# Kernel tuning notes

Measured on AMD Instinct MI355X. Metric: run time of the kernel, lower is better.

Reference implementation:

```python
import jax, jax.numpy as jnp
import numpy as np

# Static configuration (from init_kwargs)
B, T, SP = 4, 100, 20          # batch, max_time_patches, max_space_patches
S = T * SP                      # flattened seq len = 2000
H, NH = 512, 8                  # hidden size, heads
D = H // NH                     # head dim = 64
CF, CB = 4, 4                   # context_forward, context_backward
ROPE_BASE = 10000.0
NEG = -1e9


def setup_inputs() -> dict:
    key = jax.random.key(0)
    ks = jax.random.split(key, 8)
    w = 1.0 / np.sqrt(H)
    x = jax.random.normal(ks[0], (B, S, H), jnp.float32)
    # token order is space-major: timestamps = time-patch id repeated per space patch
    timestamps = jnp.broadcast_to(jnp.tile(jnp.arange(T, dtype=jnp.int32), SP), (B, S))
    attn_mask = jnp.ones((B, S), jnp.int32)
    Wq = jax.random.normal(ks[1], (H, H), jnp.float32) * w
    Wk = jax.random.normal(ks[2], (H, H), jnp.float32) * w
    Wv = jax.random.normal(ks[3], (H, H), jnp.float32) * w
    Wo = jax.random.normal(ks[4], (H, H), jnp.float32) * w
    z = jnp.zeros((H,), jnp.float32)
    return {"x": x, "attn_mask": attn_mask, "timestamps": timestamps,
            "Wq": Wq, "bq": z, "Wk": Wk, "bk": z, "Wv": Wv, "bv": z,
            "Wo": Wo, "bo": z}


def _rotate_half(u):
    return jnp.concatenate((-u[..., D // 2:], u[..., :D // 2]), axis=-1)


def _rope_tables():
    inv_freq = 1.0 / (ROPE_BASE ** (jnp.arange(0, D, 2, dtype=jnp.float32) / D))
    t = jnp.arange(T, dtype=jnp.float32)
    freqs = t[:, None] * inv_freq[None, :]          # [T, D/2]
    emb = jnp.concatenate((freqs, freqs), axis=-1)  # [T, D]
    return jnp.cos(emb), jnp.sin(emb)


def _context_mask():
    # forward/backward banded window in time, tiled over space patches
    ones = jnp.ones((T, T), jnp.float32)
    m = jnp.triu(ones, k=-CF).T          # allow up to CF future time patches
    if CB > 0:
        m = m * jnp.triu(ones, k=-CB)    # allow up to CB past time patches
    return jnp.tile(m, (SP, SP))         # [S, S]


def reference(x, attn_mask, timestamps, Wq, bq, Wk, bk, Wv, bv, Wo, bo):
    # projections -> [B, NH, S, D]
    def heads(w, b):
        return (x @ w + b).reshape(B, S, NH, D).transpose(0, 2, 1, 3)
    q, k, v = heads(Wq, bq), heads(Wk, bk), heads(Wv, bv)

    # rotary position embedding indexed by time-patch timestamps
    cos_t, sin_t = _rope_tables()
    cos = cos_t[timestamps][:, None]     # [B, 1, S, D]
    sin = sin_t[timestamps][:, None]
    q = q * cos + _rotate_half(q) * sin
    k = k * cos + _rotate_half(k) * sin

    # banded-context masked attention
    scores = jnp.einsum('bhqd,bhkd->bhqk', q, k) / jnp.sqrt(jnp.float32(D))
    mask = (_context_mask()[None, None, :, :] *
            attn_mask[:, None, None, :].astype(jnp.float32)) > 0
    scores = jnp.where(mask, scores, NEG)
    attn = jax.nn.softmax(scores, axis=-1)
    out = jnp.einsum('bhqk,bhkd->bhqd', attn, v)
    out = out.transpose(0, 2, 1, 3).reshape(B, S, H)
    return out @ Wo + bo
```

## Files before the change

### kernel.cpp

```cpp
#include <hip/hip_runtime.h>
#include <hip/hip_bf16.h>
#include <stdint.h>


typedef __bf16 bf16x8 __attribute__((ext_vector_type(8)));
typedef float f32x4 __attribute__((ext_vector_type(4)));

static const size_t O_XB = 0;
static const size_t O_WT = 8192000;
static const size_t O_Q  = 10289152;
static const size_t O_K  = 18481152;
static const size_t O_V  = 26673152;
static const size_t O_RC = 34865152;
static const size_t O_RS = 34877952;

__device__ inline void gload16(const void* g, void* l) {
  __builtin_amdgcn_global_load_lds((const __attribute__((address_space(1))) void*)g,
                                   (__attribute__((address_space(3))) void*)l, 16, 0, 0);
}

__device__ inline int xcd_swz(int orig, int nwg) {
  const int q8 = nwg >> 3, r8 = nwg & 7;
  const int xcd = orig & 7;
  return (xcd < r8 ? xcd * (q8 + 1) : r8 * (q8 + 1) + (xcd - r8) * q8) + (orig >> 3);
}

__global__ __launch_bounds__(256) void prep_kernel(
    const float* __restrict__ x, const float* __restrict__ Wq, const float* __restrict__ Wk,
    const float* __restrict__ Wv, const float* __restrict__ Wo,
    __bf16* __restrict__ xb, __bf16* __restrict__ wt,
    float* __restrict__ ropeC, float* __restrict__ ropeS)
{
  __shared__ float tile[64][65];
  const int tid = threadIdx.x;
  const int bx = blockIdx.x;
  if (bx < 4000) {
    const int idx = bx * 256 + tid;
    float4 v = ((const float4*)x)[idx];
    union { ushort4 u; __bf16 b[4]; } p;
    p.b[0] = (__bf16)v.x; p.b[1] = (__bf16)v.y; p.b[2] = (__bf16)v.z; p.b[3] = (__bf16)v.w;
    ((ushort4*)xb)[idx] = p.u;
    return;
  }
  const int wb = bx - 4000;
  const int mat = wb >> 6, sub = wb & 63;
  const int tk = (sub >> 3) * 64, tn = (sub & 7) * 64;
  const float* W = (mat == 0) ? Wq : (mat == 1) ? Wk : (mat == 2) ? Wv : Wo;
#pragma unroll
  for (int it = 0; it < 16; ++it) {
    const int idx = it * 256 + tid;
    const int kl = idx >> 6, nl = idx & 63;
    tile[kl][nl] = W[(size_t)(tk + kl) * 512 + tn + nl];
  }
  __syncthreads();
#pragma unroll
  for (int it = 0; it < 16; ++it) {
    const int idx = it * 256 + tid;
    const int nl = idx >> 6, kl = idx & 63;
    wt[(size_t)mat * 262144 + (size_t)(tn + nl) * 512 + tk + kl] = (__bf16)tile[kl][nl];
  }
  if (wb == 0) {
    for (int idx = tid; idx < 3200; idx += 256) {
      const int t = idx >> 5, i = idx & 31;
      const float f = (float)t * powf(10000.0f, -(float)i / 32.0f);
      ropeC[idx] = cosf(f);
      ropeS[idx] = sinf(f);
    }
  }
}

__device__ inline void mfma_step(const __bf16* ab, const __bf16* bb,
                                 f32x4 (&acc)[4][4], int wm, int wn, int lr, int g)
{
  bf16x8 af[4], bfr[4];
#pragma unroll
  for (int f = 0; f < 4; ++f) {
    af[f]  = *(const bf16x8*)(ab + (wm + f * 16 + lr) * 32 + g * 8);
    bfr[f] = *(const bf16x8*)(bb + (wn + f * 16 + lr) * 32 + g * 8);
  }
#pragma unroll
  for (int i = 0; i < 4; ++i)
#pragma unroll
    for (int j = 0; j < 4; ++j)
      acc[i][j] = __builtin_amdgcn_mfma_f32_16x16x32_bf16(af[i], bfr[j], acc[i][j], 0, 0, 0);
}

__device__ inline void gemm_core_p2(const __bf16* __restrict__ A, const __bf16* __restrict__ Bm,
                                    __bf16* As, __bf16* Bs, f32x4 (&acc)[4][4],
                                    int m0, int n0, int tid, int wm, int wn, int lr, int g)
{
  const int r0 = tid >> 2;
  const int aq = tid & 3;
  int gm0 = m0 + r0;      if (gm0 > 7999) gm0 = 7999;
  int gm1 = m0 + r0 + 64; if (gm1 > 7999) gm1 = 7999;
  const __bf16* a0 = A + (size_t)gm0 * 512 + aq * 8;
  const __bf16* a1 = A + (size_t)gm1 * 512 + aq * 8;
  const __bf16* b0 = Bm + (size_t)(n0 + r0) * 512 + aq * 8;
  const __bf16* b1 = Bm + (size_t)(n0 + r0 + 64) * 512 + aq * 8;

#define STAGE_QK(J, BUF) do {                                      \
    gload16(a0 + (J) * 32, As + (BUF) * 4096 + tid * 8);           \
    gload16(a1 + (J) * 32, As + (BUF) * 4096 + tid * 8 + 2048);    \
    gload16(b0 + (J) * 32, Bs + (BUF) * 4096 + tid * 8);           \
    gload16(b1 + (J) * 32, Bs + (BUF) * 4096 + tid * 8 + 2048);    \
  } while (0)

  STAGE_QK(0, 0);
  STAGE_QK(1, 1);
  __syncthreads();

  int cur = 0, st = 2;
  for (int k = 0; k < 14; ++k) {
    STAGE_QK(k + 2, st);
    mfma_step(As + cur * 4096, Bs + cur * 4096, acc, wm, wn, lr, g);
    asm volatile("s_waitcnt vmcnt(4)" ::: "memory");
    __builtin_amdgcn_s_barrier();
    __builtin_amdgcn_sched_barrier(0);
    if (++cur == 3) cur = 0;
    if (++st == 3) st = 0;
  }
  mfma_step(As + 2 * 4096, Bs + 2 * 4096, acc, wm, wn, lr, g);
  asm volatile("s_waitcnt vmcnt(0)" ::: "memory");
  __builtin_amdgcn_s_barrier();
  __builtin_amdgcn_sched_barrier(0);
  mfma_step(As, Bs, acc, wm, wn, lr, g);
#undef STAGE_QK
}

__global__ __launch_bounds__(256) void qkv_gemm(
    const __bf16* __restrict__ xb, const __bf16* __restrict__ wt,
    const float* __restrict__ bq, const float* __restrict__ bk, const float* __restrict__ bv,
    const float* __restrict__ ropeC, const float* __restrict__ ropeS,
    __bf16* __restrict__ qws, __bf16* __restrict__ kws, __bf16* __restrict__ vws)
{
  const int tid = threadIdx.x;
  const int wgid = xcd_swz(blockIdx.x, 756);
  const int mt = wgid / 12;
  const int rest = wgid - mt * 12;
  const int mat = rest >> 2;
  const int nt = rest & 3;
  const int m0 = mt * 128, n0 = nt * 128;
  __shared__ __bf16 As[12288], Bs[12288];
  __shared__ int posTbl[128];
  f32x4 acc[4][4] = {};
  const int wid = tid >> 6, lane = tid & 63;
  const int wm = (wid >> 1) << 6, wn = (wid & 1) << 6;
  const int lr = lane & 15, g = lane >> 4;

  if (tid < 128) {
    int m = m0 + tid; if (m > 7999) m = 7999;
    const int b = m / 2000;
    const int s = m - b * 2000;
    const int t = s % 100;
    const int sp = s / 100;
    posTbl[tid] = ((b * 16000 + t * 20 + sp) << 7) | t;
  }

  gemm_core_p2(xb, wt + (size_t)mat * 262144, As, Bs, acc, m0, n0, tid, wm, wn, lr, g);

  const int hn = (n0 + wn) >> 6;
  const float* bias = (mat == 0) ? bq : (mat == 1) ? bk : bv;
  __bf16* outp = (mat == 0) ? qws : (mat == 1) ? kws : vws;
  const float qscale = (mat == 0) ? 0.125f : 1.0f;

#pragma unroll
  for (int i = 0; i < 4; ++i) {
#pragma unroll
    for (int r = 0; r < 4; ++r) {
      const int row = wm + i * 16 + g * 4 + r;
      const int m = m0 + row;
      if (m >= 8000) continue;
      const int pk = posTbl[row];
      const int t = pk & 127;
      const size_t ob = ((size_t)((pk >> 7) + hn * 2000)) * 64;
      if (mat == 2) {
#pragma unroll
        for (int j = 0; j < 4; ++j) {
          float v = acc[i][j][r] + bias[n0 + wn + j * 16 + lr];
          outp[ob + j * 16 + lr] = (__bf16)v;
        }
      } else {
#pragma unroll
        for (int j = 0; j < 2; ++j) {
          const int dlo = j * 16 + lr;
          const float alo = acc[i][j][r]     + bias[n0 + wn + j * 16 + lr];
          const float ahi = acc[i][j + 2][r] + bias[n0 + wn + (j + 2) * 16 + lr];
          const float cs = ropeC[t * 32 + dlo], sn = ropeS[t * 32 + dlo];
          const float olo = (alo * cs - ahi * sn) * qscale;
          const float ohi = (ahi * cs + alo * sn) * qscale;
          outp[ob + dlo]      = (__bf16)olo;
          outp[ob + dlo + 32] = (__bf16)ohi;
        }
      }
    }
  }
}

__global__ __launch_bounds__(256) void attn_kernel(
    const __bf16* __restrict__ qw, const __bf16* __restrict__ kw, const __bf16* __restrict__ vw,
    const int* __restrict__ amask, __bf16* __restrict__ aout)
{
  const int wid = threadIdx.x >> 6, lane = threadIdx.x & 63;
  const int tid = threadIdx.x;
  const int lr = lane & 15, g = lane >> 4;
  const int tq = blockIdx.x * 4 + wid;
  const int h = blockIdx.y, b = blockIdx.z;

  int t0 = tq - 4; if (t0 < 0) t0 = 0;
  int t1 = tq + 4; if (t1 > 99) t1 = 99;
  const int k0 = t0 * 20;
  const int nk = (t1 - t0 + 1) * 20;
  const int basew = k0 & ~7;

  const int tq0 = blockIdx.x * 4;
  int t0b = tq0 - 4; if (t0b < 0) t0b = 0;
  int t1b = tq0 + 7; if (t1b > 99) t1b = 99;
  const int kb0 = (t0b * 20) & ~7;
  const int nks = (t1b + 1) * 20 - kb0;
  const int woff = basew - kb0;

  __shared__ __bf16 Vs[64][264];
  __shared__ __bf16 Pl[4][20][200];
  __shared__ float addm[4][192];

  const size_t hb = (size_t)(b * 8 + h) * 2000;
  const __bf16* qp = qw + (hb + (size_t)tq * 20) * 64;
  const __bf16* vp = vw + (hb + (size_t)kb0) * 64;

  for (int k = lane; k < 192; k += 64) {
    const int kg = basew + k;
    float v = -1e9f;
    if (kg >= k0 && kg < k0 + nk) {
      const int tk = kg / 20;
      const int spk = kg - tk * 20;
      if (amask[b * 2000 + spk * 100 + tk] != 0) v = 0.0f;
    }
    addm[wid][k] = v;
  }

  for (int idx = tid; idx < 264 * 16; idx += 256) {
    const int pr = idx >> 4, d4 = (idx & 15) * 4;
    union { ushort4 u; __bf16 e[4]; } p;
    p.u = make_ushort4(0, 0, 0, 0);
    if (pr < nks) p.u = *(const ushort4*)(vp + (size_t)pr * 64 + d4);
    Vs[d4 + 0][pr] = p.e[0];
    Vs[d4 + 1][pr] = p.e[1];
    Vs[d4 + 2][pr] = p.e[2];
    Vs[d4 + 3][pr] = p.e[3];
  }

  bf16x8 qf[2][2];
#pragma unroll
  for (int jq = 0; jq < 2; ++jq) {
    int q = jq * 16 + lr; if (q > 19) q = 19;
#pragma unroll
    for (int ks = 0; ks < 2; ++ks)
      qf[jq][ks] = *(const bf16x8*)(qp + q * 64 + ks * 32 + g * 8);
  }

  f32x4 acc[12][2] = {};
  __builtin_amdgcn_s_setprio(1);
#pragma unroll
  for (int i = 0; i < 12; ++i) {
    int krow = basew + i * 16 + lr; if (krow > 1999) krow = 1999;
    const __bf16* kr = kw + (hb + (size_t)krow) * 64;
    const bf16x8 af0 = *(const bf16x8*)(kr + g * 8);
    const bf16x8 af1 = *(const bf16x8*)(kr + 32 + g * 8);
    acc[i][0] = __builtin_amdgcn_mfma_f32_16x16x32_bf16(af0, qf[0][0], acc[i][0], 0, 0, 0);
    acc[i][0] = __builtin_amdgcn_mfma_f32_16x16x32_bf16(af1, qf[0][1], acc[i][0], 0, 0, 0);
    acc[i][1] = __builtin_amdgcn_mfma_f32_16x16x32_bf16(af0, qf[1][0], acc[i][1], 0, 0, 0);
    acc[i][1] = __builtin_amdgcn_mfma_f32_16x16x32_bf16(af1, qf[1][1], acc[i][1], 0, 0, 0);
  }
  __builtin_amdgcn_s_setprio(0);

  __syncthreads();

#pragma unroll
  for (int jq = 0; jq < 2; ++jq) {
    float mx = -1e30f;
#pragma unroll
    for (int i = 0; i < 12; ++i)
#pragma unroll
      for (int r = 0; r < 4; ++r) {
        acc[i][jq][r] += addm[wid][i * 16 + g * 4 + r];
        mx = fmaxf(mx, acc[i][jq][r]);
      }
    mx = fmaxf(mx, __shfl_xor(mx, 16));
    mx = fmaxf(mx, __shfl_xor(mx, 32));
    float sm = 0.0f;
#pragma unroll
    for (int i = 0; i < 12; ++i)
#pragma unroll
      for (int r = 0; r < 4; ++r) {
        const float p = __expf(acc[i][jq][r] - mx);
        acc[i][jq][r] = p;
        sm += p;
      }
    sm += __shfl_xor(sm, 16);
    sm += __shfl_xor(sm, 32);
    const float rinv = 1.0f / sm;
    const int q = jq * 16 + lr;
    if (q < 20) {
#pragma unroll
      for (int i = 0; i < 12; ++i) {
        union { ushort4 u; __bf16 e[4]; } pk;
        pk.e[0] = (__bf16)(acc[i][jq][0] * rinv);
        pk.e[1] = (__bf16)(acc[i][jq][1] * rinv);
        pk.e[2] = (__bf16)(acc[i][jq][2] * rinv);
        pk.e[3] = (__bf16)(acc[i][jq][3] * rinv);
        *(ushort4*)&Pl[wid][q][i * 16 + g * 4] = pk.u;
      }
    }
  }

  __syncthreads();

  f32x4 acc2[2][4] = {};
  __builtin_amdgcn_s_setprio(1);
#pragma unroll
  for (int kb = 0; kb < 6; ++kb) {
    const int kvloc = woff + kb * 32 + g * 8;
    bf16x8 bfv[4];
#pragma unroll
    for (int j2 = 0; j2 < 4; ++j2)
      bfv[j2] = *(const bf16x8*)&Vs[j2 * 16 + lr][kvloc];
#pragma unroll
    for (int i2 = 0; i2 < 2; ++i2) {
      int qr = i2 * 16 + lr; if (qr > 19) qr = 19;
      const bf16x8 pa = *(const bf16x8*)&Pl[wid][qr][kb * 32 + g * 8];
#pragma unroll
      for (int j2 = 0; j2 < 4; ++j2)
        acc2[i2][j2] = __builtin_amdgcn_mfma_f32_16x16x32_bf16(pa, bfv[j2], acc2[i2][j2], 0, 0, 0);
    }
  }
  __builtin_amdgcn_s_setprio(0);

#pragma unroll
  for (int i2 = 0; i2 < 2; ++i2)
#pragma unroll
    for (int r = 0; r < 4; ++r) {
      const int q = i2 * 16 + g * 4 + r;
      if (q < 20) {
        const size_t ob = ((size_t)b * 2000 + q * 100 + tq) * 512 + h * 64;
#pragma unroll
        for (int j2 = 0; j2 < 4; ++j2)
          aout[ob + j2 * 16 + lr] = (__bf16)acc2[i2][j2][r];
      }
    }
}

__global__ __launch_bounds__(256) void out_gemm(
    const __bf16* __restrict__ ab, const __bf16* __restrict__ wot,
    const float* __restrict__ bo, float* __restrict__ out)
{
  const int tid = threadIdx.x;
  const int wgid = xcd_swz(blockIdx.x, 252);
  const int mt = wgid >> 2, nt = wgid & 3;
  const int m0 = mt * 128, n0 = nt * 128;
  __shared__ __bf16 As[12288], Bs[12288];
  f32x4 acc[4][4] = {};
  const int wid = tid >> 6, lane = tid & 63;
  const int wm = (wid >> 1) << 6, wn = (wid & 1) << 6;
  const int lr = lane & 15, g = lane >> 4;

  gemm_core_p2(ab, wot, As, Bs, acc, m0, n0, tid, wm, wn, lr, g);

#pragma unroll
  for (int i = 0; i < 4; ++i) {
#pragma unroll
    for (int r = 0; r < 4; ++r) {
      const int m = m0 + wm + i * 16 + g * 4 + r;
      if (m < 8000) {
#pragma unroll
        for (int j = 0; j < 4; ++j) {
          const int n = n0 + wn + j * 16 + lr;
          out[(size_t)m * 512 + n] = acc[i][j][r] + bo[n];
        }
      }
    }
  }
}

extern "C" void kernel_launch(void* const* d_in, const int* in_sizes, int n_in,
                              void* d_out, int out_size, void* d_ws, size_t ws_size,
                              hipStream_t stream) {
  const float* x   = (const float*)d_in[0];
  const int* amask = (const int*)d_in[1];
  const float* Wq = (const float*)d_in[3];
  const float* bq = (const float*)d_in[4];
  const float* Wk = (const float*)d_in[5];
  const float* bk = (const float*)d_in[6];
  const float* Wv = (const float*)d_in[7];
  const float* bv = (const float*)d_in[8];
  const float* Wo = (const float*)d_in[9];
  const float* bo = (const float*)d_in[10];
  float* out = (float*)d_out;

  char* ws = (char*)d_ws;
  __bf16* xb    = (__bf16*)(ws + O_XB);
  __bf16* wt    = (__bf16*)(ws + O_WT);
  __bf16* qws   = (__bf16*)(ws + O_Q);
  __bf16* kws   = (__bf16*)(ws + O_K);
  __bf16* vws   = (__bf16*)(ws + O_V);
  float*  ropeC = (float*)(ws + O_RC);
  float*  ropeS = (float*)(ws + O_RS);
  __bf16* aout  = (__bf16*)(ws + O_XB);

  prep_kernel<<<4256, 256, 0, stream>>>(x, Wq, Wk, Wv, Wo, xb, wt, ropeC, ropeS);
  qkv_gemm<<<756, 256, 0, stream>>>(xb, wt, bq, bk, bv, ropeC, ropeS, qws, kws, vws);
  attn_kernel<<<dim3(25, 8, 4), 256, 0, stream>>>(qws, kws, vws, amask, aout);
  out_gemm<<<252, 256, 0, stream>>>(aout, wt + 3 * 262144, bo, out);
}
```

Baseline: 88.08 us.

## Fuse Q/K/V projections per A tile and widen output GEMM tiles

The QKV GEMM now loads each 64-row activation tile once and multiplies it against all three weight matrices, using 500 workgroups instead of 756 that each reloaded the A tile for one matrix. The output GEMM switches to 128x256 tiles with 126 workgroups. Both drop the 3-stage pipeline with partial vmcnt waits in favour of simple double buffering with a full barrier per k-step. That may expose more load latency, and the smaller grids (126 blocks for out_gemm) may underfill the 256 CUs.

```diff
diff --git a/kernel.cpp b/kernel.cpp
--- a/kernel.cpp
+++ b/kernel.cpp
@@ -69,86 +69,26 @@
   }
 }
 
-__device__ inline void mfma_step(const __bf16* ab, const __bf16* bb,
-                                 f32x4 (&acc)[4][4], int wm, int wn, int lr, int g)
-{
-  bf16x8 af[4], bfr[4];
-#pragma unroll
-  for (int f = 0; f < 4; ++f) {
-    af[f]  = *(const bf16x8*)(ab + (wm + f * 16 + lr) * 32 + g * 8);
-    bfr[f] = *(const bf16x8*)(bb + (wn + f * 16 + lr) * 32 + g * 8);
-  }
-#pragma unroll
-  for (int i = 0; i < 4; ++i)
-#pragma unroll
-    for (int j = 0; j < 4; ++j)
-      acc[i][j] = __builtin_amdgcn_mfma_f32_16x16x32_bf16(af[i], bfr[j], acc[i][j], 0, 0, 0);
-}
-
-__device__ inline void gemm_core_p2(const __bf16* __restrict__ A, const __bf16* __restrict__ Bm,
-                                    __bf16* As, __bf16* Bs, f32x4 (&acc)[4][4],
-                                    int m0, int n0, int tid, int wm, int wn, int lr, int g)
-{
-  const int r0 = tid >> 2;
-  const int aq = tid & 3;
-  int gm0 = m0 + r0;      if (gm0 > 7999) gm0 = 7999;
-  int gm1 = m0 + r0 + 64; if (gm1 > 7999) gm1 = 7999;
-  const __bf16* a0 = A + (size_t)gm0 * 512 + aq * 8;
-  const __bf16* a1 = A + (size_t)gm1 * 512 + aq * 8;
-  const __bf16* b0 = Bm + (size_t)(n0 + r0) * 512 + aq * 8;
-  const __bf16* b1 = Bm + (size_t)(n0 + r0 + 64) * 512 + aq * 8;
-
-#define STAGE_QK(J, BUF) do {                                      \
-    gload16(a0 + (J) * 32, As + (BUF) * 4096 + tid * 8);           \
-    gload16(a1 + (J) * 32, As + (BUF) * 4096 + tid * 8 + 2048);    \
-    gload16(b0 + (J) * 32, Bs + (BUF) * 4096 + tid * 8);           \
-    gload16(b1 + (J) * 32, Bs + (BUF) * 4096 + tid * 8 + 2048);    \
-  } while (0)
-
-  STAGE_QK(0, 0);
-  STAGE_QK(1, 1);
-  __syncthreads();
-
-  int cur = 0, st = 2;
-  for (int k = 0; k < 14; ++k) {
-    STAGE_QK(k + 2, st);
-    mfma_step(As + cur * 4096, Bs + cur * 4096, acc, wm, wn, lr, g);
-    asm volatile("s_waitcnt vmcnt(4)" ::: "memory");
-    __builtin_amdgcn_s_barrier();
-    __builtin_amdgcn_sched_barrier(0);
-    if (++cur == 3) cur = 0;
-    if (++st == 3) st = 0;
-  }
-  mfma_step(As + 2 * 4096, Bs + 2 * 4096, acc, wm, wn, lr, g);
-  asm volatile("s_waitcnt vmcnt(0)" ::: "memory");
-  __builtin_amdgcn_s_barrier();
-  __builtin_amdgcn_sched_barrier(0);
-  mfma_step(As, Bs, acc, wm, wn, lr, g);
-#undef STAGE_QK
-}
-
-__global__ __launch_bounds__(256) void qkv_gemm(
+__global__ __launch_bounds__(256) void qkv_fused(
     const __bf16* __restrict__ xb, const __bf16* __restrict__ wt,
     const float* __restrict__ bq, const float* __restrict__ bk, const float* __restrict__ bv,
     const float* __restrict__ ropeC, const float* __restrict__ ropeS,
     __bf16* __restrict__ qws, __bf16* __restrict__ kws, __bf16* __restrict__ vws)
 {
   const int tid = threadIdx.x;
-  const int wgid = xcd_swz(blockIdx.x, 756);
-  const int mt = wgid / 12;
-  const int rest = wgid - mt * 12;
-  const int mat = rest >> 2;
-  const int nt = rest & 3;
-  const int m0 = mt * 128, n0 = nt * 128;
-  __shared__ __bf16 As[12288], Bs[12288];
-  __shared__ int posTbl[128];
-  f32x4 acc[4][4] = {};
+  const int wgid = xcd_swz(blockIdx.x, 500);
+  const int mt = wgid >> 2, nt = wgid & 3;
+  const int m0 = mt * 64, n0 = nt * 128;
+  __shared__ __bf16 As[2 * 2048];
+  __shared__ __bf16 Bs[2 * 3 * 4096];
+  __shared__ int posTbl[64];
+  f32x4 acc[3][2][4] = {};
   const int wid = tid >> 6, lane = tid & 63;
-  const int wm = (wid >> 1) << 6, wn = (wid & 1) << 6;
+  const int wm = (wid >> 1) << 5, wn = (wid & 1) << 6;
   const int lr = lane & 15, g = lane >> 4;
 
-  if (tid < 128) {
-    int m = m0 + tid; if (m > 7999) m = 7999;
+  if (tid < 64) {
+    const int m = m0 + tid;
     const int b = m / 2000;
     const int s = m - b * 2000;
     const int t = s % 100;
@@ -156,40 +96,80 @@
     posTbl[tid] = ((b * 16000 + t * 20 + sp) << 7) | t;
   }
 
-  gemm_core_p2(xb, wt + (size_t)mat * 262144, As, Bs, acc, m0, n0, tid, wm, wn, lr, g);
+  const __bf16* a_src = xb + (size_t)(m0 + (tid >> 2)) * 512 + (tid & 3) * 8;
+
+#define STG(BUF, KK) do {                                                        \
+    gload16(a_src + (KK), As + (BUF) * 2048 + tid * 8);                          \
+    _Pragma("unroll")                                                            \
+    for (int mm = 0; mm < 3; ++mm)                                               \
+      _Pragma("unroll")                                                          \
+      for (int jj = 0; jj < 2; ++jj) {                                           \
+        const int c = tid + jj * 256;                                            \
+        gload16(wt + (size_t)mm * 262144 + (size_t)(n0 + (c >> 2)) * 512 + (KK)  \
+                    + (c & 3) * 8,                                               \
+                Bs + ((BUF) * 3 + mm) * 4096 + c * 8);                           \
+      }                                                                          \
+  } while (0)
+
+  STG(0, 0);
+  __syncthreads();
+
+  int cur = 0;
+  for (int kks = 0; kks < 16; ++kks) {
+    if (kks < 15) STG(cur ^ 1, (kks + 1) * 32);
+    bf16x8 af[2];
+#pragma unroll
+    for (int f = 0; f < 2; ++f)
+      af[f] = *(const bf16x8*)(As + cur * 2048 + (wm + f * 16 + lr) * 32 + g * 8);
+#pragma unroll
+    for (int mat = 0; mat < 3; ++mat) {
+      bf16x8 bfr[4];
+#pragma unroll
+      for (int f = 0; f < 4; ++f)
+        bfr[f] = *(const bf16x8*)(Bs + (cur * 3 + mat) * 4096 + (wn + f * 16 + lr) * 32 + g * 8);
+#pragma unroll
+      for (int i = 0; i < 2; ++i)
+#pragma unroll
+        for (int j = 0; j < 4; ++j)
+          acc[mat][i][j] = __builtin_amdgcn_mfma_f32_16x16x32_bf16(af[i], bfr[j], acc[mat][i][j], 0, 0, 0);
+    }
+    __syncthreads();
+    cur ^= 1;
+  }
+#undef STG
 
   const int hn = (n0 + wn) >> 6;
-  const float* bias = (mat == 0) ? bq : (mat == 1) ? bk : bv;
-  __bf16* outp = (mat == 0) ? qws : (mat == 1) ? kws : vws;
-  const float qscale = (mat == 0) ? 0.125f : 1.0f;
-
-#pragma unroll
-  for (int i = 0; i < 4; ++i) {
-#pragma unroll
-    for (int r = 0; r < 4; ++r) {
-      const int row = wm + i * 16 + g * 4 + r;
-      const int m = m0 + row;
-      if (m >= 8000) continue;
-      const int pk = posTbl[row];
-      const int t = pk & 127;
-      const size_t ob = ((size_t)((pk >> 7) + hn * 2000)) * 64;
-      if (mat == 2) {
-#pragma unroll
-        for (int j = 0; j < 4; ++j) {
-          float v = acc[i][j][r] + bias[n0 + wn + j * 16 + lr];
-          outp[ob + j * 16 + lr] = (__bf16)v;
-        }
-      } else {
-#pragma unroll
-        for (int j = 0; j < 2; ++j) {
-          const int dlo = j * 16 + lr;
-          const float alo = acc[i][j][r]     + bias[n0 + wn + j * 16 + lr];
-          const float ahi = acc[i][j + 2][r] + bias[n0 + wn + (j + 2) * 16 + lr];
-          const float cs = ropeC[t * 32 + dlo], sn = ropeS[t * 32 + dlo];
-          const float olo = (alo * cs - ahi * sn) * qscale;
-          const float ohi = (ahi * cs + alo * sn) * qscale;
-          outp[ob + dlo]      = (__bf16)olo;
-          outp[ob + dlo + 32] = (__bf16)ohi;
+#pragma unroll
+  for (int mat = 0; mat < 3; ++mat) {
+    const float* bias = (mat == 0) ? bq : (mat == 1) ? bk : bv;
+    __bf16* outp = (mat == 0) ? qws : (mat == 1) ? kws : vws;
+    const float qscale = (mat == 0) ? 0.125f : 1.0f;
+#pragma unroll
+    for (int i = 0; i < 2; ++i) {
+#pragma unroll
+      for (int r = 0; r < 4; ++r) {
+        const int row = wm + i * 16 + g * 4 + r;
+        const int pk = posTbl[row];
+        const int t = pk & 127;
+        const size_t ob = ((size_t)((pk >> 7) + hn * 2000)) * 64;
+        if (mat == 2) {
+#pragma unroll
+          for (int j = 0; j < 4; ++j) {
+            float v = acc[mat][i][j][r] + bias[n0 + wn + j * 16 + lr];
+            outp[ob + j * 16 + lr] = (__bf16)v;
+          }
+        } else {
+#pragma unroll
+          for (int j = 0; j < 2; ++j) {
+            const int dlo = j * 16 + lr;
+            const float alo = acc[mat][i][j][r]     + bias[n0 + wn + j * 16 + lr];
+            const float ahi = acc[mat][i][j + 2][r] + bias[n0 + wn + (j + 2) * 16 + lr];
+            const float cs = ropeC[t * 32 + dlo], sn = ropeS[t * 32 + dlo];
+            const float olo = (alo * cs - ahi * sn) * qscale;
+            const float ohi = (ahi * cs + alo * sn) * qscale;
+            outp[ob + dlo]      = (__bf16)olo;
+            outp[ob + dlo + 32] = (__bf16)ohi;
+          }
         }
       }
     }
@@ -354,16 +334,53 @@
     const float* __restrict__ bo, float* __restrict__ out)
 {
   const int tid = threadIdx.x;
-  const int wgid = xcd_swz(blockIdx.x, 252);
-  const int mt = wgid >> 2, nt = wgid & 3;
-  const int m0 = mt * 128, n0 = nt * 128;
-  __shared__ __bf16 As[12288], Bs[12288];
-  f32x4 acc[4][4] = {};
+  const int wgid = xcd_swz(blockIdx.x, 126);
+  const int mt = wgid >> 1, nt = wgid & 1;
+  const int m0 = mt * 128, n0 = nt * 256;
+  __shared__ __bf16 As[2 * 4096];
+  __shared__ __bf16 Bs[2 * 8192];
+  f32x4 acc[4][8] = {};
   const int wid = tid >> 6, lane = tid & 63;
-  const int wm = (wid >> 1) << 6, wn = (wid & 1) << 6;
+  const int wm = (wid >> 1) << 6, wn = (wid & 1) << 7;
   const int lr = lane & 15, g = lane >> 4;
 
-  gemm_core_p2(ab, wot, As, Bs, acc, m0, n0, tid, wm, wn, lr, g);
+#define STG2(BUF, KK) do {                                                       \
+    _Pragma("unroll")                                                            \
+    for (int jj = 0; jj < 2; ++jj) {                                             \
+      const int c = tid + jj * 256;                                              \
+      int row = m0 + (c >> 2); if (row > 7999) row = 7999;                       \
+      gload16(ab + (size_t)row * 512 + (KK) + (c & 3) * 8,                       \
+              As + (BUF) * 4096 + c * 8);                                        \
+    }                                                                            \
+    _Pragma("unroll")                                                            \
+    for (int jj = 0; jj < 4; ++jj) {                                             \
+      const int c = tid + jj * 256;                                              \
+      gload16(wot + (size_t)(n0 + (c >> 2)) * 512 + (KK) + (c & 3) * 8,          \
+              Bs + (BUF) * 8192 + c * 8);                                        \
+    }                                                                            \
+  } while (0)
+
+  STG2(0, 0);
+  __syncthreads();
+
+  int cur = 0;
+  for (int kks = 0; kks < 16; ++kks) {
+    if (kks < 15) STG2(cur ^ 1, (kks + 1) * 32);
+    bf16x8 af[4];
+#pragma unroll
+    for (int f = 0; f < 4; ++f)
+      af[f] = *(const bf16x8*)(As + cur * 4096 + (wm + f * 16 + lr) * 32 + g * 8);
+#pragma unroll
+    for (int j = 0; j < 8; ++j) {
+      const bf16x8 bfr = *(const bf16x8*)(Bs + cur * 8192 + (wn + j * 16 + lr) * 32 + g * 8);
+#pragma unroll
+      for (int i = 0; i < 4; ++i)
+        acc[i][j] = __builtin_amdgcn_mfma_f32_16x16x32_bf16(af[i], bfr, acc[i][j], 0, 0, 0);
+    }
+    __syncthreads();
+    cur ^= 1;
+  }
+#undef STG2
 
 #pragma unroll
   for (int i = 0; i < 4; ++i) {
@@ -372,7 +389,7 @@
       const int m = m0 + wm + i * 16 + g * 4 + r;
       if (m < 8000) {
 #pragma unroll
-        for (int j = 0; j < 4; ++j) {
+        for (int j = 0; j < 8; ++j) {
           const int n = n0 + wn + j * 16 + lr;
           out[(size_t)m * 512 + n] = acc[i][j][r] + bo[n];
         }
@@ -407,7 +424,7 @@
   __bf16* aout  = (__bf16*)(ws + O_XB);
 
   prep_kernel<<<4256, 256, 0, stream>>>(x, Wq, Wk, Wv, Wo, xb, wt, ropeC, ropeS);
-  qkv_gemm<<<756, 256, 0, stream>>>(xb, wt, bq, bk, bv, ropeC, ropeS, qws, kws, vws);
+  qkv_fused<<<500, 256, 0, stream>>>(xb, wt, bq, bk, bv, ropeC, ropeS, qws, kws, vws);
   attn_kernel<<<dim3(25, 8, 4), 256, 0, stream>>>(qws, kws, vws, amask, aout);
-  out_gemm<<<252, 256, 0, stream>>>(aout, wt + 3 * 262144, bo, out);
-}
+  out_gemm<<<126, 256, 0, stream>>>(aout, wt + 3 * 262144, bo, out);
+}
```

After: 98.57 us. 11.9% more time.
